# Kernel tuning notes

Hardware: AMD Instinct MI355X
Metric: run time of the kernel (lower is better)

## Reference

```python
import jax, jax.numpy as jnp
import numpy as np

N, D_IN, D_P, N_HEADS, N_CTRS, D_OUT = 8192, 256, 64, 8, 128, 256


def setup_inputs() -> dict:
    key = jax.random.key(0)
    k = jax.random.split(key, 6)
    x = jax.random.normal(k[0], (N, D_IN), dtype=jnp.float32)
    ctrs = jax.random.normal(k[1], (N_HEADS, N_CTRS, D_P), dtype=jnp.float32) * 0.5
    Wv = jax.random.normal(k[2], (N_HEADS, N_CTRS, D_P, D_P), dtype=jnp.float32) * 0.02
    Ov = jax.random.normal(k[3], (N_HEADS, N_CTRS, D_P), dtype=jnp.float32) * 0.02
    Wq = jax.random.normal(k[4], (D_IN, D_P, N_HEADS), dtype=jnp.float32) * 0.05
    Wo = jax.random.normal(k[5], (N_HEADS * D_P, D_OUT), dtype=jnp.float32) * 0.02
    return {"x": x, "ctrs": ctrs, "Wv": Wv, "Ov": Ov, "Wq": Wq, "Wo": Wo}


def reference(x, ctrs, Wv, Ov, Wq, Wo):
    # project input per head: (N,d_in) x (d_in,d_p,h) -> (h,N,d_p)
    x_in = jnp.einsum('ni,iph->hnp', x, Wq)
    # RBF soft assignments over centroids: (h,N,c)
    dist_sq = jnp.sum((x_in[:, :, None, :] - ctrs[:, None, :, :]) ** 2, axis=-1)
    assignments = jax.nn.softmax(-dist_sq, axis=2)
    # soft-weighted per-cluster matrices: (h,N,g,p)
    scored_weights = jnp.einsum('hnc,hcgp->hngp', assignments, Wv)
    # soft-weighted offsets: (h,N,p)
    scored_offsets = jnp.einsum('hnc,hcp->hnp', assignments, Ov)
    # elementwise multiply (broadcast over g) then reduce over g, as in original
    heads_out = jnp.sum(scored_weights * x_in[:, :, None, :], axis=2) + scored_offsets
    # NOTE: original reshapes (h,N,p) directly into (N, h*p) in row-major order
    heads_out = heads_out.reshape(x.shape[0], N_HEADS * D_P)
    return heads_out @ Wo
```

## Files before the change

### kernel.cpp

```cpp
#include <hip/hip_runtime.h>
#include <math.h>

#define NROWS 8192
#define DIN   256
#define NH    8
#define NC    128
#define DOUT  256

typedef unsigned short ushort_t;
typedef __attribute__((ext_vector_type(8))) short bf16x8;
typedef __attribute__((ext_vector_type(4))) float f32x4;
typedef __attribute__((ext_vector_type(8))) unsigned short u16x8;

static __device__ __forceinline__ ushort_t f2bf(float f) {
  union { float f; unsigned u; } v; v.f = f;
  unsigned r = v.u + 0x7fffu + ((v.u >> 16) & 1u);
  return (ushort_t)(r >> 16);
}
static __device__ __forceinline__ float bf2f(ushort_t h) {
  union { unsigned u; float f; } v; v.u = ((unsigned)h) << 16;
  return v.f;
}

#define MFMA16(a, b, c) __builtin_amdgcn_mfma_f32_16x16x32_bf16((a), (b), (c), 0, 0, 0)
#define GLOAD_LDS16(g, l)                                                     \
  __builtin_amdgcn_global_load_lds(                                           \
      (const __attribute__((address_space(1))) void*)(g),                     \
      (__attribute__((address_space(3))) void*)(l), 16, 0, 0)

__global__ __launch_bounds__(256) void prep_kernel(
    const float* __restrict__ Wq, const float* __restrict__ ctrs,
    const float* __restrict__ Wo, const float* __restrict__ Wv,
    const float* __restrict__ Ov, ushort_t* __restrict__ wcvtT,
    ushort_t* __restrict__ ctr3T, float* __restrict__ cbias,
    ushort_t* __restrict__ WoT, ushort_t* __restrict__ W2bT) {
  int bid = blockIdx.x;
  int t = threadIdx.x;
  if (bid < 512) {
    int j = bid, k = t;
    int h = j >> 6, p = j & 63;
    float v = Wq[((size_t)k * 64 + p) * 8 + h];
    ushort_t hi = f2bf(v), lo = f2bf(v - bf2f(hi));
    wcvtT[(size_t)j * 512 + k]       = hi;
    wcvtT[(size_t)j * 512 + 256 + k] = lo;
  } else if (bid < 768) {
    int idx = (bid - 512) * 4 + (t >> 6);
    int p = t & 63;
    float v = ctrs[(size_t)idx * 64 + p];
    float sq = v * v;
    #pragma unroll
    for (int off = 32; off >= 1; off >>= 1) sq += __shfl_xor(sq, off, 64);
    if (p == 0) cbias[idx] = -sq;
    ushort_t hi = f2bf(v), lo = f2bf(v - bf2f(hi));
    ctr3T[(size_t)idx * 192 + p]       = hi;
    ctr3T[(size_t)idx * 192 + 64 + p]  = lo;
    ctr3T[(size_t)idx * 192 + 128 + p] = hi;
  } else if (bid < 1280) {
    int k = bid - 768;
    int n = t;
    WoT[(size_t)n * 512 + k] = f2bf(Wo[(size_t)k * 256 + n]);
  } else {
    int b = (bid - 1280) * 4 + (t >> 6);
    int p = t & 63;
    int h = b >> 7, c = b & 127;
    const float* wv = Wv + (size_t)b * 4096;
    float acc = 0.f;
    #pragma unroll 8
    for (int g = 0; g < 64; ++g) acc += wv[g * 64 + p];
    W2bT[((size_t)h * 128 + p) * 128 + c]      = f2bf(acc);
    W2bT[((size_t)h * 128 + 64 + p) * 128 + c] = f2bf(Ov[(size_t)b * 64 + p]);
  }
}

__global__ __launch_bounds__(256) void gemm2_kernel(
    const ushort_t* __restrict__ A, const ushort_t* __restrict__ Bt,
    float* __restrict__ out) {
  __shared__ ushort_t At[64 * 64];
  __shared__ ushort_t Bl[64 * 64];
  const int t = threadIdx.x;
  const int w = t >> 6, l = t & 63;
  const int wr = w >> 1, wc = w & 1;
  const int m0 = (blockIdx.x >> 2) * 64, n0 = (blockIdx.x & 3) * 64;
  const int lr = l & 15, lk = l >> 4;

  f32x4 acc[2][2];
  #pragma unroll
  for (int a = 0; a < 2; ++a)
    #pragma unroll
    for (int b = 0; b < 2; ++b) acc[a][b] = (f32x4){0.f, 0.f, 0.f, 0.f};

  for (int k0 = 0; k0 < 512; k0 += 64) {
    #pragma unroll
    for (int i = 0; i < 2; ++i) {
      int q = (i * 4 + w) * 64 + l;
      int row = q >> 3, s = q & 7;
      int kl = k0 + ((s ^ (row & 7)) << 3);
      GLOAD_LDS16(A + (size_t)(m0 + row) * 512 + kl,
                  (char*)At + (size_t)(i * 4 + w) * 1024);
    }
    #pragma unroll
    for (int i = 0; i < 2; ++i) {
      int q = (i * 4 + w) * 64 + l;
      int row = q >> 3, s = q & 7;
      int kl = k0 + ((s ^ (row & 7)) << 3);
      GLOAD_LDS16(Bt + (size_t)(n0 + row) * 512 + kl,
                  (char*)Bl + (size_t)(i * 4 + w) * 1024);
    }
    __syncthreads();
    #pragma unroll
    for (int kk = 0; kk < 2; ++kk) {
      bf16x8 af[2], bfr[2];
      #pragma unroll
      for (int a = 0; a < 2; ++a) {
        int row = wr * 32 + a * 16 + lr;
        int s = (kk * 4 + lk) ^ (row & 7);
        af[a] = *(const bf16x8*)((const char*)At + row * 128 + s * 16);
      }
      #pragma unroll
      for (int b = 0; b < 2; ++b) {
        int row = wc * 32 + b * 16 + lr;
        int s = (kk * 4 + lk) ^ (row & 7);
        bfr[b] = *(const bf16x8*)((const char*)Bl + row * 128 + s * 16);
      }
      #pragma unroll
      for (int a = 0; a < 2; ++a)
        #pragma unroll
        for (int b = 0; b < 2; ++b)
          acc[a][b] = MFMA16(af[a], bfr[b], acc[a][b]);
    }
    __syncthreads();
  }
  #pragma unroll
  for (int a = 0; a < 2; ++a) {
    #pragma unroll
    for (int b = 0; b < 2; ++b) {
      #pragma unroll
      for (int r = 0; r < 4; ++r) {
        int rowg = m0 + wr * 32 + a * 16 + lk * 4 + r;
        int colg = n0 + wc * 32 + b * 16 + lr;
        out[(size_t)rowg * 256 + colg] = acc[a][b][r];
      }
    }
  }
}

__global__ __launch_bounds__(256, 2) void fused_pair_kernel(
    const float* __restrict__ x,
    const ushort_t* __restrict__ wcvtT,
    const ushort_t* __restrict__ ctr3T,
    const float* __restrict__ cbias,
    const ushort_t* __restrict__ W2bT,
    ushort_t* __restrict__ ho2) {
  __shared__ __align__(16) char Au_raw[36864];
  __shared__ char B0lds[16384];
  __shared__ char B1lds[16384];
  __shared__ float cb_lds[128];

  ushort_t* Axh = (ushort_t*)Au_raw;
  ushort_t* Axl = (ushort_t*)(Au_raw + 18432);
  ushort_t* A1  = (ushort_t*)Au_raw;
  ushort_t* A2  = (ushort_t*)Au_raw;

  const int t = threadIdx.x;
  const int w = t >> 6, l = t & 63;
  const int lr = l & 15, lk = l >> 4;
  const int h = blockIdx.x >> 6;
  const int n0 = (blockIdx.x & 63) * 128;

#define STAGE_B(BUF, SRC, LDB, KOFF)                                          \
  {                                                                           \
    _Pragma("unroll")                                                         \
    for (int i = 0; i < 4; ++i) {                                             \
      int q = (i * 4 + w) * 64 + l;                                           \
      int row = q >> 3, s = q & 7;                                            \
      GLOAD_LDS16((SRC) + (size_t)(h * 128 + row) * (LDB) + (KOFF) +          \
                      ((s ^ (row & 7)) << 3),                                 \
                  (char*)(BUF) + (size_t)(i * 4 + w) * 1024);                 \
    }                                                                         \
  }

#define STAGE_BX(BUF, KC)                                                     \
  {                                                                           \
    _Pragma("unroll")                                                         \
    for (int i = 0; i < 4; ++i) {                                             \
      int q = (i * 4 + w) * 64 + l;                                           \
      int row = q >> 3, s = q & 7;                                            \
      int sw = (s ^ (row & 7)) << 3;                                          \
      int jj = h * 64 + (row & 63);                                           \
      int koff = (row < 64 ? 0 : 256) + (KC) * 64 + sw;                       \
      GLOAD_LDS16(wcvtT + (size_t)jj * 512 + koff,                            \
                  (char*)(BUF) + (size_t)(i * 4 + w) * 1024);                 \
    }                                                                         \
  }

#define MFMA_STEP(BUF, ACC0, ACC1, KBASE, ASPLIT)                             \
  {                                                                           \
    _Pragma("unroll")                                                         \
    for (int kk = 0; kk < 2; ++kk) {                                          \
      int klog = (KBASE) + kk * 32 + lk * 8;                                  \
      int kp = (ASPLIT) ? (klog < 64 ? klog : klog - 64) : klog;              \
      bf16x8 af0 = *(const bf16x8*)&A1[(w * 16 + lr) * 136 + kp];             \
      bf16x8 af1 = *(const bf16x8*)&A1[(64 + w * 16 + lr) * 136 + kp];        \
      _Pragma("unroll")                                                       \
      for (int cj = 0; cj < 8; ++cj) {                                        \
        int brow = cj * 16 + lr;                                              \
        int slot = (kk * 4 + lk) ^ (brow & 7);                                \
        bf16x8 bfr =                                                          \
            *(const bf16x8*)((const char*)(BUF) + brow * 128 + slot * 16);    \
        (ACC0)[cj] = MFMA16(af0, bfr, (ACC0)[cj]);                            \
        (ACC1)[cj] = MFMA16(af1, bfr, (ACC1)[cj]);                            \
      }                                                                       \
    }                                                                         \
  }

#define MFMAX(BUF)                                                            \
  {                                                                           \
    _Pragma("unroll")                                                         \
    for (int kk = 0; kk < 2; ++kk) {                                          \
      bf16x8 ah0 = *(const bf16x8*)&Axh[(w * 16 + lr) * 72 + kk * 32 + lk * 8];     \
      bf16x8 al0 = *(const bf16x8*)&Axl[(w * 16 + lr) * 72 + kk * 32 + lk * 8];     \
      bf16x8 ah1 = *(const bf16x8*)&Axh[(64 + w * 16 + lr) * 72 + kk * 32 + lk * 8];\
      bf16x8 al1 = *(const bf16x8*)&Axl[(64 + w * 16 + lr) * 72 + kk * 32 + lk * 8];\
      _Pragma("unroll")                                                       \
      for (int cj = 0; cj < 4; ++cj) {                                        \
        int rh = cj * 16 + lr;                                                \
        int slot = (kk * 4 + lk) ^ (rh & 7);                                  \
        bf16x8 bh = *(const bf16x8*)((const char*)(BUF) + rh * 128 + slot * 16);\
        bf16x8 bl = *(const bf16x8*)((const char*)(BUF) + (64 + rh) * 128 + slot * 16);\
        acc_x0[cj] = MFMA16(ah0, bh, acc_x0[cj]);                             \
        acc_x0[cj] = MFMA16(al0, bh, acc_x0[cj]);                             \
        acc_x0[cj] = MFMA16(ah0, bl, acc_x0[cj]);                             \
        acc_x1[cj] = MFMA16(ah1, bh, acc_x1[cj]);                             \
        acc_x1[cj] = MFMA16(al1, bh, acc_x1[cj]);                             \
        acc_x1[cj] = MFMA16(ah1, bl, acc_x1[cj]);                             \
      }                                                                       \
    }                                                                         \
  }

#define BAR() __builtin_amdgcn_s_barrier()
#define SCHED() __builtin_amdgcn_sched_barrier(0)
#define DRAIN_LGKM()                                                          \
  { asm volatile("s_waitcnt lgkmcnt(0)" ::: "memory"); SCHED(); }

  const int xrow = t >> 2;
  const int xseg = (t & 3) << 4;
  const float* xb0 = x + (size_t)(n0 + xrow) * 256 + xseg;
  const float* xb1 = xb0 + 64 * 256;
  float4 xr[8];

#define LOAD_X(KC)                                                            \
  {                                                                           \
    _Pragma("unroll")                                                         \
    for (int j = 0; j < 4; ++j) xr[j]     = *(const float4*)(xb0 + (KC) * 64 + j * 4); \
    _Pragma("unroll")                                                         \
    for (int j = 0; j < 4; ++j) xr[4 + j] = *(const float4*)(xb1 + (KC) * 64 + j * 4); \
  }

#define CVT_AX()                                                              \
  {                                                                           \
    _Pragma("unroll")                                                         \
    for (int hf = 0; hf < 2; ++hf) {                                          \
      u16x8 hv0, hv1, lv0, lv1;                                               \
      _Pragma("unroll")                                                       \
      for (int j = 0; j < 2; ++j) {                                           \
        float f4[8] = {xr[hf*4 + j*2].x, xr[hf*4 + j*2].y, xr[hf*4 + j*2].z,  \
                       xr[hf*4 + j*2].w, xr[hf*4 + j*2 + 1].x,                \
                       xr[hf*4 + j*2 + 1].y, xr[hf*4 + j*2 + 1].z,            \
                       xr[hf*4 + j*2 + 1].w};                                 \
        _Pragma("unroll")                                                     \
        for (int e = 0; e < 8; ++e) {                                         \
          ushort_t hi = f2bf(f4[e]);                                          \
          if (j == 0) { hv0[e] = hi; lv0[e] = f2bf(f4[e] - bf2f(hi)); }       \
          else        { hv1[e] = hi; lv1[e] = f2bf(f4[e] - bf2f(hi)); }       \
        }                                                                     \
      }                                                                       \
      int ro = hf * 64 + xrow;                                                \
      *(u16x8*)&Axh[ro * 72 + xseg]     = hv0;                                \
      *(u16x8*)&Axh[ro * 72 + xseg + 8] = hv1;                                \
      *(u16x8*)&Axl[ro * 72 + xseg]     = lv0;                                \
      *(u16x8*)&Axl[ro * 72 + xseg + 8] = lv1;                                \
    }                                                                         \
  }

#define SOFTMAX(ACC, ROFF)                                                    \
  {                                                                           \
    float cbv[8];                                                             \
    _Pragma("unroll")                                                         \
    for (int cj = 0; cj < 8; ++cj) cbv[cj] = cb_lds[cj * 16 + lr];            \
    _Pragma("unroll")                                                         \
    for (int r = 0; r < 4; ++r) {                                             \
      float v[8];                                                             \
      float m = -1e30f;                                                       \
      _Pragma("unroll")                                                       \
      for (int cj = 0; cj < 8; ++cj) {                                        \
        v[cj] = 2.f * (ACC)[cj][r] + cbv[cj];                                 \
        m = fmaxf(m, v[cj]);                                                  \
      }                                                                       \
      m = fmaxf(m, __shfl_xor(m, 1, 64));                                     \
      m = fmaxf(m, __shfl_xor(m, 2, 64));                                     \
      m = fmaxf(m, __shfl_xor(m, 4, 64));                                     \
      m = fmaxf(m, __shfl_xor(m, 8, 64));                                     \
      float s = 0.f;                                                          \
      _Pragma("unroll")                                                       \
      for (int cj = 0; cj < 8; ++cj) {                                        \
        v[cj] = __expf(v[cj] - m);                                            \
        s += v[cj];                                                           \
      }                                                                       \
      s += __shfl_xor(s, 1, 64);                                              \
      s += __shfl_xor(s, 2, 64);                                              \
      s += __shfl_xor(s, 4, 64);                                              \
      s += __shfl_xor(s, 8, 64);                                              \
      float inv = 1.f / s;                                                    \
      int row = (ROFF) + w * 16 + lk * 4 + r;                                 \
      _Pragma("unroll")                                                       \
      for (int cj = 0; cj < 8; ++cj)                                          \
        A2[row * 136 + cj * 16 + lr] = f2bf(v[cj] * inv);                     \
    }                                                                         \
  }

  cb_lds[t & 127] = cbias[h * 128 + (t & 127)];
  LOAD_X(0);
  STAGE_BX(B0lds, 0);
  SCHED();
  STAGE_BX(B1lds, 1);
  SCHED();
  f32x4 acc_x0[4], acc_x1[4];
  #pragma unroll
  for (int cj = 0; cj < 4; ++cj) {
    acc_x0[cj] = (f32x4){0.f, 0.f, 0.f, 0.f};
    acc_x1[cj] = (f32x4){0.f, 0.f, 0.f, 0.f};
  }
  CVT_AX();
  SCHED();
  LOAD_X(1);
  asm volatile("s_waitcnt vmcnt(12)" ::: "memory");
  DRAIN_LGKM(); BAR(); SCHED();
  MFMAX(B0lds);
  DRAIN_LGKM(); BAR(); SCHED();
  STAGE_BX(B0lds, 2);
  SCHED();
  CVT_AX();
  SCHED();
  LOAD_X(2);
  DRAIN_LGKM(); BAR(); SCHED();
  MFMAX(B1lds);
  DRAIN_LGKM(); BAR(); SCHED();
  STAGE_BX(B1lds, 3);
  SCHED();
  CVT_AX();
  SCHED();
  LOAD_X(3);
  DRAIN_LGKM(); BAR(); SCHED();
  MFMAX(B0lds);
  DRAIN_LGKM(); BAR(); SCHED();
  STAGE_B(B0lds, ctr3T, 192, 0);
  SCHED();
  CVT_AX();
  DRAIN_LGKM(); BAR(); SCHED();
  MFMAX(B1lds);
  DRAIN_LGKM(); BAR(); SCHED();

  STAGE_B(B1lds, ctr3T, 192, 64);
  #pragma unroll
  for (int cj = 0; cj < 4; ++cj) {
    #pragma unroll
    for (int r = 0; r < 4; ++r) {
      int row = w * 16 + lk * 4 + r;
      int p = cj * 16 + lr;
      float v0 = acc_x0[cj][r];
      ushort_t hi0 = f2bf(v0);
      A1[row * 136 + p] = hi0;
      A1[row * 136 + 64 + p] = f2bf(v0 - bf2f(hi0));
      float v1 = acc_x1[cj][r];
      ushort_t hi1 = f2bf(v1);
      A1[(64 + row) * 136 + p] = hi1;
      A1[(64 + row) * 136 + 64 + p] = f2bf(v1 - bf2f(hi1));
    }
  }
  asm volatile("s_waitcnt vmcnt(4)" ::: "memory");
  DRAIN_LGKM(); BAR(); SCHED();

  f32x4 acc0[8], acc1[8];
  #pragma unroll
  for (int cj = 0; cj < 8; ++cj) {
    acc0[cj] = (f32x4){0.f, 0.f, 0.f, 0.f};
    acc1[cj] = (f32x4){0.f, 0.f, 0.f, 0.f};
  }
  MFMA_STEP(B0lds, acc0, acc1, 0, 1);
  DRAIN_LGKM(); BAR(); SCHED();
  STAGE_B(B0lds, ctr3T, 192, 128);
  asm volatile("s_waitcnt vmcnt(4)" ::: "memory");
  BAR(); SCHED();
  MFMA_STEP(B1lds, acc0, acc1, 64, 1);
  DRAIN_LGKM(); BAR(); SCHED();
  STAGE_B(B1lds, W2bT, 128, 0);
  asm volatile("s_waitcnt vmcnt(4)" ::: "memory");
  BAR(); SCHED();
  MFMA_STEP(B0lds, acc0, acc1, 128, 1);
  DRAIN_LGKM();

  SOFTMAX(acc0, 0);
  SOFTMAX(acc1, 64);
  DRAIN_LGKM();
  BAR(); SCHED();

  f32x4 accT0[8], accT1[8];
  #pragma unroll
  for (int cj = 0; cj < 8; ++cj) {
    accT0[cj] = (f32x4){0.f, 0.f, 0.f, 0.f};
    accT1[cj] = (f32x4){0.f, 0.f, 0.f, 0.f};
  }
  STAGE_B(B0lds, W2bT, 128, 64);
  asm volatile("s_waitcnt vmcnt(4)" ::: "memory");
  BAR(); SCHED();
  {
    MFMA_STEP(B1lds, accT0, accT1, 0, 0);
  }
  DRAIN_LGKM();
  asm volatile("s_waitcnt vmcnt(0)" ::: "memory");
  BAR(); SCHED();
  MFMA_STEP(B0lds, accT0, accT1, 64, 0);

  #pragma unroll
  for (int cj = 0; cj < 4; ++cj) {
    #pragma unroll
    for (int r = 0; r < 4; ++r) {
      int row = w * 16 + lk * 4 + r;
      int p = cj * 16 + lr;
      float hov0 = acc_x0[cj][r] * accT0[cj][r] + accT0[cj + 4][r];
      ((ushort_t*)B1lds)[row * 64 + p] = f2bf(hov0);
      float hov1 = acc_x1[cj][r] * accT1[cj][r] + accT1[cj + 4][r];
      ((ushort_t*)B1lds)[(64 + row) * 64 + p] = f2bf(hov1);
    }
  }
  DRAIN_LGKM(); BAR(); SCHED();
  #pragma unroll
  for (int i = 0; i < 4; ++i) {
    int q = i * 256 + t;
    int row = q >> 3, s = q & 7;
    uint4 v = *(const uint4*)((const char*)B1lds + row * 128 + s * 16);
    *(uint4*)(ho2 + ((size_t)h * NROWS + n0 + row) * 64 + s * 8) = v;
  }
#undef STAGE_B
#undef STAGE_BX
#undef MFMA_STEP
#undef MFMAX
#undef BAR
#undef SCHED
#undef DRAIN_LGKM
#undef LOAD_X
#undef CVT_AX
#undef SOFTMAX
}

extern "C" void kernel_launch(void* const* d_in, const int* in_sizes, int n_in,
                              void* d_out, int out_size, void* d_ws, size_t ws_size,
                              hipStream_t stream) {
  (void)in_sizes; (void)n_in; (void)out_size; (void)ws_size;
  const float* x    = (const float*)d_in[0];
  const float* ctrs = (const float*)d_in[1];
  const float* Wv   = (const float*)d_in[2];
  const float* Ov   = (const float*)d_in[3];
  const float* Wq   = (const float*)d_in[4];
  const float* Wo   = (const float*)d_in[5];
  float* out = (float*)d_out;

  char* wsb = (char*)d_ws;
  ushort_t* wcvtT = (ushort_t*)wsb;
  ushort_t* ctr3T = (ushort_t*)(wsb + 524288);
  float*    cb    = (float*)   (wsb + 917504);
  ushort_t* W2bT  = (ushort_t*)(wsb + 921600);
  ushort_t* WoT   = (ushort_t*)(wsb + 1183744);
  ushort_t* ho2   = (ushort_t*)(wsb + 2097152);

  prep_kernel<<<1536, 256, 0, stream>>>(Wq, ctrs, Wo, Wv, Ov,
                                        wcvtT, ctr3T, cb, WoT, W2bT);
  fused_pair_kernel<<<512, 256, 0, stream>>>(x, wcvtT, ctr3T, cb, W2bT, ho2);
  gemm2_kernel<<<512, 256, 0, stream>>>(ho2, WoT, out);
}
```

Before: 43.33 us.

## Fuse output projection GEMM into fused_pair kernel, drop separate gemm2 launch

The output projection by Wo is now computed inside the fused kernel. Because of the row-major reshape quirk, each block's 128x64 head tile maps to 16 output rows with K=512, so the block multiplies its tile directly against WoT with MFMA and writes fp32 output. This removes the ho2 intermediate write/read and the second kernel launch. In exchange, WoT fragments are loaded straight from global memory with no LDS staging, and the LDS write of the tile now uses an XOR-swizzled layout.

```diff
diff --git a/kernel.cpp b/kernel.cpp
--- a/kernel.cpp
+++ b/kernel.cpp
@@ -72,85 +72,14 @@
   }
 }
 
-__global__ __launch_bounds__(256) void gemm2_kernel(
-    const ushort_t* __restrict__ A, const ushort_t* __restrict__ Bt,
-    float* __restrict__ out) {
-  __shared__ ushort_t At[64 * 64];
-  __shared__ ushort_t Bl[64 * 64];
-  const int t = threadIdx.x;
-  const int w = t >> 6, l = t & 63;
-  const int wr = w >> 1, wc = w & 1;
-  const int m0 = (blockIdx.x >> 2) * 64, n0 = (blockIdx.x & 3) * 64;
-  const int lr = l & 15, lk = l >> 4;
-
-  f32x4 acc[2][2];
-  #pragma unroll
-  for (int a = 0; a < 2; ++a)
-    #pragma unroll
-    for (int b = 0; b < 2; ++b) acc[a][b] = (f32x4){0.f, 0.f, 0.f, 0.f};
-
-  for (int k0 = 0; k0 < 512; k0 += 64) {
-    #pragma unroll
-    for (int i = 0; i < 2; ++i) {
-      int q = (i * 4 + w) * 64 + l;
-      int row = q >> 3, s = q & 7;
-      int kl = k0 + ((s ^ (row & 7)) << 3);
-      GLOAD_LDS16(A + (size_t)(m0 + row) * 512 + kl,
-                  (char*)At + (size_t)(i * 4 + w) * 1024);
-    }
-    #pragma unroll
-    for (int i = 0; i < 2; ++i) {
-      int q = (i * 4 + w) * 64 + l;
-      int row = q >> 3, s = q & 7;
-      int kl = k0 + ((s ^ (row & 7)) << 3);
-      GLOAD_LDS16(Bt + (size_t)(n0 + row) * 512 + kl,
-                  (char*)Bl + (size_t)(i * 4 + w) * 1024);
-    }
-    __syncthreads();
-    #pragma unroll
-    for (int kk = 0; kk < 2; ++kk) {
-      bf16x8 af[2], bfr[2];
-      #pragma unroll
-      for (int a = 0; a < 2; ++a) {
-        int row = wr * 32 + a * 16 + lr;
-        int s = (kk * 4 + lk) ^ (row & 7);
-        af[a] = *(const bf16x8*)((const char*)At + row * 128 + s * 16);
-      }
-      #pragma unroll
-      for (int b = 0; b < 2; ++b) {
-        int row = wc * 32 + b * 16 + lr;
-        int s = (kk * 4 + lk) ^ (row & 7);
-        bfr[b] = *(const bf16x8*)((const char*)Bl + row * 128 + s * 16);
-      }
-      #pragma unroll
-      for (int a = 0; a < 2; ++a)
-        #pragma unroll
-        for (int b = 0; b < 2; ++b)
-          acc[a][b] = MFMA16(af[a], bfr[b], acc[a][b]);
-    }
-    __syncthreads();
-  }
-  #pragma unroll
-  for (int a = 0; a < 2; ++a) {
-    #pragma unroll
-    for (int b = 0; b < 2; ++b) {
-      #pragma unroll
-      for (int r = 0; r < 4; ++r) {
-        int rowg = m0 + wr * 32 + a * 16 + lk * 4 + r;
-        int colg = n0 + wc * 32 + b * 16 + lr;
-        out[(size_t)rowg * 256 + colg] = acc[a][b][r];
-      }
-    }
-  }
-}
-
 __global__ __launch_bounds__(256, 2) void fused_pair_kernel(
     const float* __restrict__ x,
     const ushort_t* __restrict__ wcvtT,
     const ushort_t* __restrict__ ctr3T,
     const float* __restrict__ cbias,
     const ushort_t* __restrict__ W2bT,
-    ushort_t* __restrict__ ho2) {
+    const ushort_t* __restrict__ WoT,
+    float* __restrict__ out) {
   __shared__ __align__(16) char Au_raw[36864];
   __shared__ char B0lds[16384];
   __shared__ char B1lds[16384];
@@ -413,9 +342,7 @@
   STAGE_B(B0lds, W2bT, 128, 64);
   asm volatile("s_waitcnt vmcnt(4)" ::: "memory");
   BAR(); SCHED();
-  {
-    MFMA_STEP(B1lds, accT0, accT1, 0, 0);
-  }
+  MFMA_STEP(B1lds, accT0, accT1, 0, 0);
   DRAIN_LGKM();
   asm volatile("s_waitcnt vmcnt(0)" ::: "memory");
   BAR(); SCHED();
@@ -425,21 +352,44 @@
   for (int cj = 0; cj < 4; ++cj) {
     #pragma unroll
     for (int r = 0; r < 4; ++r) {
-      int row = w * 16 + lk * 4 + r;
-      int p = cj * 16 + lr;
+      int row0 = w * 16 + lk * 4 + r;
+      int slotp = cj * 2 + (lr >> 3);
+      int sw = (slotp ^ ((row0 >> 3) & 7));
       float hov0 = acc_x0[cj][r] * accT0[cj][r] + accT0[cj + 4][r];
-      ((ushort_t*)B1lds)[row * 64 + p] = f2bf(hov0);
+      *(ushort_t*)((char*)B1lds + row0 * 128 + sw * 16 + (lr & 7) * 2) =
+          f2bf(hov0);
       float hov1 = acc_x1[cj][r] * accT1[cj][r] + accT1[cj + 4][r];
-      ((ushort_t*)B1lds)[(64 + row) * 64 + p] = f2bf(hov1);
+      *(ushort_t*)((char*)B1lds + (64 + row0) * 128 + sw * 16 + (lr & 7) * 2) =
+          f2bf(hov1);
     }
   }
   DRAIN_LGKM(); BAR(); SCHED();
-  #pragma unroll
-  for (int i = 0; i < 4; ++i) {
-    int q = i * 256 + t;
-    int row = q >> 3, s = q & 7;
-    uint4 v = *(const uint4*)((const char*)B1lds + row * 128 + s * 16);
-    *(uint4*)(ho2 + ((size_t)h * NROWS + n0 + row) * 64 + s * 8) = v;
+
+  {
+    const int vbase = (h << 10) + (blockIdx.x & 63) * 16;
+    f32x4 accO[4];
+    #pragma unroll
+    for (int c = 0; c < 4; ++c) accO[c] = (f32x4){0.f, 0.f, 0.f, 0.f};
+    #pragma unroll
+    for (int ks = 0; ks < 16; ++ks) {
+      int rowt = 8 * lr + (ks >> 1);
+      int slot = (((ks & 1) * 4 + lk) ^ (lr & 7));
+      bf16x8 af = *(const bf16x8*)((const char*)B1lds + rowt * 128 + slot * 16);
+      #pragma unroll
+      for (int c = 0; c < 4; ++c) {
+        int n = (w * 4 + c) * 16 + lr;
+        bf16x8 bfr = *(const bf16x8*)(WoT + (size_t)n * 512 + ks * 32 + lk * 8);
+        accO[c] = MFMA16(af, bfr, accO[c]);
+      }
+    }
+    #pragma unroll
+    for (int c = 0; c < 4; ++c) {
+      #pragma unroll
+      for (int r = 0; r < 4; ++r) {
+        out[(size_t)(vbase + lk * 4 + r) * 256 + (w * 4 + c) * 16 + lr] =
+            accO[c][r];
+      }
+    }
   }
 #undef STAGE_B
 #undef STAGE_BX
@@ -471,10 +421,9 @@
   float*    cb    = (float*)   (wsb + 917504);
   ushort_t* W2bT  = (ushort_t*)(wsb + 921600);
   ushort_t* WoT   = (ushort_t*)(wsb + 1183744);
-  ushort_t* ho2   = (ushort_t*)(wsb + 2097152);
 
   prep_kernel<<<1536, 256, 0, stream>>>(Wq, ctrs, Wo, Wv, Ov,
                                         wcvtT, ctr3T, cb, WoT, W2bT);
-  fused_pair_kernel<<<512, 256, 0, stream>>>(x, wcvtT, ctr3T, cb, W2bT, ho2);
-  gemm2_kernel<<<512, 256, 0, stream>>>(ho2, WoT, out);
+  fused_pair_kernel<<<512, 256, 0, stream>>>(x, wcvtT, ctr3T, cb, W2bT, WoT,
+                                             out);
 }
```

Result: slower. 45.40 us (+4.8%).

## Restructure staging pipeline to one barrier per stage with full waits

Applied to the files above, without the earlier changes.

Reorders the double-buffered LDS staging so each stage issues the next buffer's global-to-LDS copy and the next x load, then runs MFMAs on the current buffer and the conversion, and ends with one combined vmcnt(0)/lgkmcnt(0) wait plus barrier. This replaces the previous pattern of two barriers per step with partial vmcnt counts. The aim is to halve barrier count and overlap loads with compute more simply. In exchange, waiting on vmcnt(0) at every stage removes the deeper prefetch slack the partial-count waits allowed.

```diff
diff --git a/kernel.cpp b/kernel.cpp
--- a/kernel.cpp
+++ b/kernel.cpp
@@ -239,8 +239,11 @@
 
 #define BAR() __builtin_amdgcn_s_barrier()
 #define SCHED() __builtin_amdgcn_sched_barrier(0)
-#define DRAIN_LGKM()                                                          \
-  { asm volatile("s_waitcnt lgkmcnt(0)" ::: "memory"); SCHED(); }
+#define WAITALL_BAR()                                                         \
+  {                                                                           \
+    asm volatile("s_waitcnt vmcnt(0) lgkmcnt(0)" ::: "memory");               \
+    SCHED(); BAR(); SCHED();                                                  \
+  }
 
   const int xrow = t >> 2;
   const int xseg = (t & 3) << 4;
@@ -319,11 +322,8 @@
   }
 
   cb_lds[t & 127] = cbias[h * 128 + (t & 127)];
+  STAGE_BX(B0lds, 0);
   LOAD_X(0);
-  STAGE_BX(B0lds, 0);
-  SCHED();
-  STAGE_BX(B1lds, 1);
-  SCHED();
   f32x4 acc_x0[4], acc_x1[4];
   #pragma unroll
   for (int cj = 0; cj < 4; ++cj) {
@@ -331,34 +331,26 @@
     acc_x1[cj] = (f32x4){0.f, 0.f, 0.f, 0.f};
   }
   CVT_AX();
-  SCHED();
+  WAITALL_BAR();
+
+  STAGE_BX(B1lds, 1);
   LOAD_X(1);
-  asm volatile("s_waitcnt vmcnt(12)" ::: "memory");
-  DRAIN_LGKM(); BAR(); SCHED();
   MFMAX(B0lds);
-  DRAIN_LGKM(); BAR(); SCHED();
+  CVT_AX();
+  WAITALL_BAR();
   STAGE_BX(B0lds, 2);
-  SCHED();
+  LOAD_X(2);
+  MFMAX(B1lds);
   CVT_AX();
-  SCHED();
-  LOAD_X(2);
-  DRAIN_LGKM(); BAR(); SCHED();
+  WAITALL_BAR();
+  STAGE_BX(B1lds, 3);
+  LOAD_X(3);
+  MFMAX(B0lds);
+  CVT_AX();
+  WAITALL_BAR();
+  STAGE_B(B0lds, ctr3T, 192, 0);
   MFMAX(B1lds);
-  DRAIN_LGKM(); BAR(); SCHED();
-  STAGE_BX(B1lds, 3);
-  SCHED();
-  CVT_AX();
-  SCHED();
-  LOAD_X(3);
-  DRAIN_LGKM(); BAR(); SCHED();
-  MFMAX(B0lds);
-  DRAIN_LGKM(); BAR(); SCHED();
-  STAGE_B(B0lds, ctr3T, 192, 0);
-  SCHED();
-  CVT_AX();
-  DRAIN_LGKM(); BAR(); SCHED();
-  MFMAX(B1lds);
-  DRAIN_LGKM(); BAR(); SCHED();
+  WAITALL_BAR();
 
   STAGE_B(B1lds, ctr3T, 192, 64);
   #pragma unroll
@@ -377,9 +369,6 @@
       A1[(64 + row) * 136 + 64 + p] = f2bf(v1 - bf2f(hi1));
     }
   }
-  asm volatile("s_waitcnt vmcnt(4)" ::: "memory");
-  DRAIN_LGKM(); BAR(); SCHED();
-
   f32x4 acc0[8], acc1[8];
   #pragma unroll
   for (int cj = 0; cj < 8; ++cj) {
@@ -387,40 +376,25 @@
     acc1[cj] = (f32x4){0.f, 0.f, 0.f, 0.f};
   }
   MFMA_STEP(B0lds, acc0, acc1, 0, 1);
-  DRAIN_LGKM(); BAR(); SCHED();
+  WAITALL_BAR();
   STAGE_B(B0lds, ctr3T, 192, 128);
-  asm volatile("s_waitcnt vmcnt(4)" ::: "memory");
-  BAR(); SCHED();
   MFMA_STEP(B1lds, acc0, acc1, 64, 1);
-  DRAIN_LGKM(); BAR(); SCHED();
+  WAITALL_BAR();
   STAGE_B(B1lds, W2bT, 128, 0);
-  asm volatile("s_waitcnt vmcnt(4)" ::: "memory");
-  BAR(); SCHED();
   MFMA_STEP(B0lds, acc0, acc1, 128, 1);
-  DRAIN_LGKM();
-
+  WAITALL_BAR();
+  STAGE_B(B0lds, W2bT, 128, 64);
   SOFTMAX(acc0, 0);
   SOFTMAX(acc1, 64);
-  DRAIN_LGKM();
-  BAR(); SCHED();
-
   f32x4 accT0[8], accT1[8];
   #pragma unroll
   for (int cj = 0; cj < 8; ++cj) {
     accT0[cj] = (f32x4){0.f, 0.f, 0.f, 0.f};
     accT1[cj] = (f32x4){0.f, 0.f, 0.f, 0.f};
   }
-  STAGE_B(B0lds, W2bT, 128, 64);
-  asm volatile("s_waitcnt vmcnt(4)" ::: "memory");
-  BAR(); SCHED();
-  {
-    MFMA_STEP(B1lds, accT0, accT1, 0, 0);
-  }
-  DRAIN_LGKM();
-  asm volatile("s_waitcnt vmcnt(0)" ::: "memory");
-  BAR(); SCHED();
+  MFMA_STEP(B1lds, accT0, accT1, 0, 0);
+  WAITALL_BAR();
   MFMA_STEP(B0lds, accT0, accT1, 64, 0);
-
   #pragma unroll
   for (int cj = 0; cj < 4; ++cj) {
     #pragma unroll
@@ -433,7 +407,8 @@
       ((ushort_t*)B1lds)[(64 + row) * 64 + p] = f2bf(hov1);
     }
   }
-  DRAIN_LGKM(); BAR(); SCHED();
+  asm volatile("s_waitcnt lgkmcnt(0)" ::: "memory");
+  SCHED(); BAR(); SCHED();
   #pragma unroll
   for (int i = 0; i < 4; ++i) {
     int q = i * 256 + t;
@@ -447,7 +422,7 @@
 #undef MFMAX
 #undef BAR
 #undef SCHED
-#undef DRAIN_LGKM
+#undef WAITALL_BAR
 #undef LOAD_X
 #undef CVT_AX
 #undef SOFTMAX
```

Result: no change. 42.91 us (-1.0%).
